# Kernel optimization log

Measured on AMD Instinct MI355X. Metric: run time of the kernel, lower is better.

## Reference

```python
import jax, jax.numpy as jnp
import numpy as np

THETA = 10000.0


def _apply_rope(xh, positions, theta):
    # xh: [B, H, S, d_k]; positions: [S] int
    d_k = xh.shape[-1]
    inv_freq = theta ** (-jnp.arange(0, d_k, 2, dtype=jnp.float32) / d_k)  # [d_k/2]
    angles = positions.astype(jnp.float32)[:, None] * inv_freq[None, :]     # [S, d_k/2]
    cos = jnp.cos(angles)
    sin = jnp.sin(angles)
    x1 = xh[..., 0::2]
    x2 = xh[..., 1::2]
    r1 = x1 * cos - x2 * sin
    r2 = x1 * sin + x2 * cos
    return jnp.stack([r1, r2], axis=-1).reshape(xh.shape)


def setup_inputs() -> dict:
    key = jax.random.key(0)
    ks = jax.random.split(key, 5)
    B, S, D = 2, 2048, 1024
    std = np.sqrt(1.0 / D).astype(np.float32)
    return {
        "x": jax.random.normal(ks[0], (B, S, D), dtype=jnp.float32),
        "token_positions": jnp.arange(S, dtype=jnp.int64 if jax.config.jax_enable_x64 else jnp.int32),
        "Wq": jax.random.normal(ks[1], (D, D), dtype=jnp.float32) * std,
        "Wk": jax.random.normal(ks[2], (D, D), dtype=jnp.float32) * std,
        "Wv": jax.random.normal(ks[3], (D, D), dtype=jnp.float32) * std,
        "Wo": jax.random.normal(ks[4], (D, D), dtype=jnp.float32) * std,
    }


def reference(x, token_positions, Wq, Wk, Wv, Wo):
    B, S, D = x.shape
    n_heads = 16
    d_k = D // n_heads

    # QKV projections (torch does x @ W.T)
    q = x @ Wq.T
    k = x @ Wk.T
    v = x @ Wv.T

    def split_heads(t):  # [B,S,D] -> [B,H,S,d_k]
        return t.reshape(B, S, n_heads, d_k).transpose(0, 2, 1, 3)

    qh = _apply_rope(split_heads(q), token_positions, THETA)
    kh = _apply_rope(split_heads(k), token_positions, THETA)
    vh = split_heads(v)

    scores = jnp.einsum("bhqd,bhkd->bhqk", qh, kh) / jnp.sqrt(jnp.float32(d_k))
    causal = jnp.tril(jnp.ones((S, S), dtype=bool))
    scores = jnp.where(causal, scores, -jnp.inf)
    attn = jax.nn.softmax(scores, axis=-1)

    out_h = jnp.einsum("bhqk,bhkd->bhqd", attn, vh)  # [B,H,S,d_k]
    out = out_h.transpose(0, 2, 1, 3).reshape(B, S, D)
    return out @ Wo.T
```

## Files before the change

### kernel.cpp

```cpp
#include <hip/hip_runtime.h>

typedef unsigned int u32;
typedef __attribute__((ext_vector_type(8))) short short8;
typedef __attribute__((ext_vector_type(4))) float f32x4;

__device__ __forceinline__ unsigned short f2bf(float f) {
  union { float f; u32 u; } x; x.f = f;
  u32 u = x.u;
  return (unsigned short)((u + 0x7fffu + ((u >> 16) & 1u)) >> 16);
}
__device__ __forceinline__ float bf2f(unsigned short b) {
  union { u32 u; float f; } x; x.u = ((u32)b) << 16;
  return x.f;
}
__device__ __forceinline__ f32x4 mfma_bf16(short8 a, short8 b, f32x4 c) {
  return __builtin_amdgcn_mfma_f32_16x16x32_bf16(a, b, c, 0, 0, 0);
}

typedef __attribute__((address_space(3))) unsigned int lds_u32;
typedef const __attribute__((address_space(1))) unsigned int glb_u32;
__device__ __forceinline__ void gload_lds16(const unsigned short* g, unsigned short* l) {
  __builtin_amdgcn_global_load_lds((glb_u32*)g, (lds_u32*)l, 16, 0, 0);
}

__global__ __launch_bounds__(256) void cvt_kernel(const float* __restrict__ src,
                                                  unsigned short* __restrict__ dst, int n4) {
  int i = blockIdx.x * 256 + threadIdx.x;
  if (i >= n4) return;
  float4 v = ((const float4*)src)[i];
  ushort4 o;
  o.x = f2bf(v.x); o.y = f2bf(v.y); o.z = f2bf(v.z); o.w = f2bf(v.w);
  ((ushort4*)dst)[i] = o;
}

__global__ __launch_bounds__(256) void cvt_w_kernel(const float* __restrict__ wq,
                                                    const float* __restrict__ wk,
                                                    const float* __restrict__ wv,
                                                    const float* __restrict__ wo,
                                                    unsigned short* __restrict__ dqkv,
                                                    unsigned short* __restrict__ dwo) {
  const int i = blockIdx.x * 256 + threadIdx.x;
  const int w = blockIdx.y;
  const float* src = (w == 0) ? wq : (w == 1) ? wk : (w == 2) ? wv : wo;
  unsigned short* dst = (w == 3) ? dwo : dqkv + (size_t)w * 1048576;
  float4 v = ((const float4*)src)[i];
  ushort4 o;
  o.x = f2bf(v.x); o.y = f2bf(v.y); o.z = f2bf(v.z); o.w = f2bf(v.w);
  ((ushort4*)dst)[i] = o;
}

__global__ __launch_bounds__(256) void gemm_qkv(const unsigned short* __restrict__ A,
                                                const unsigned short* __restrict__ B,
                                                unsigned short* __restrict__ qk,
                                                unsigned short* __restrict__ kk,
                                                unsigned short* __restrict__ vtm) {
  constexpr int K = 1024;
  __shared__ unsigned short As[128 * 32];
  __shared__ unsigned short Bs[128 * 32];
  const int tid = threadIdx.x;
  const int wave = tid >> 6, lane = tid & 63;
  const int l15 = lane & 15, quad = lane >> 4;
  const int wr = wave >> 1, wc = wave & 1;
  const int m0 = blockIdx.y * 128, n0 = blockIdx.x * 128;
  f32x4 acc[4][4] = {};
  const int srow = wave * 32 + (lane >> 2);
  const int scol = (lane & 3) * 8;
  const unsigned short* Ag0 = A + (size_t)(m0 + srow) * K + scol;
  const unsigned short* Ag1 = A + (size_t)(m0 + srow + 16) * K + scol;
  const unsigned short* Bg0 = B + (size_t)(n0 + srow) * K + scol;
  const unsigned short* Bg1 = B + (size_t)(n0 + srow + 16) * K + scol;
  unsigned short* Al0 = &As[wave * 1024];
  unsigned short* Al1 = &As[wave * 1024 + 512];
  unsigned short* Bl0 = &Bs[wave * 1024];
  unsigned short* Bl1 = &Bs[wave * 1024 + 512];
  for (int k0 = 0; k0 < K; k0 += 32) {
    __syncthreads();
    gload_lds16(Ag0 + k0, Al0);
    gload_lds16(Ag1 + k0, Al1);
    gload_lds16(Bg0 + k0, Bl0);
    gload_lds16(Bg1 + k0, Bl1);
    __syncthreads();
    short8 a[4], b[4];
#pragma unroll
    for (int i = 0; i < 4; ++i) a[i] = *(const short8*)&As[(wr * 64 + i * 16 + l15) * 32 + quad * 8];
#pragma unroll
    for (int j = 0; j < 4; ++j) b[j] = *(const short8*)&Bs[(wc * 64 + j * 16 + l15) * 32 + quad * 8];
#pragma unroll
    for (int i = 0; i < 4; ++i)
#pragma unroll
      for (int j = 0; j < 4; ++j) acc[i][j] = mfma_bf16(a[i], b[j], acc[i][j]);
  }
  const int proj = n0 >> 10;
  const int nn0 = (n0 & 1023) + wc * 64;
  if (proj < 2) {
    unsigned short* dst = (proj == 0) ? qk : kk;
#pragma unroll
    for (int i = 0; i < 4; ++i) {
      const int mb = m0 + wr * 64 + i * 16 + quad * 4;
#pragma unroll
      for (int j = 0; j < 4; ++j) {
        const int nn = nn0 + j * 16 + l15;
#pragma unroll
        for (int r = 0; r < 4; ++r) dst[(size_t)(mb + r) * 1024 + nn] = f2bf(acc[i][j][r]);
      }
    }
  } else {
#pragma unroll
    for (int i = 0; i < 4; ++i) {
      const int mb = m0 + wr * 64 + i * 16 + quad * 4;
      const int bb = mb >> 11, s = mb & 2047;
#pragma unroll
      for (int j = 0; j < 4; ++j) {
        const int nn = nn0 + j * 16 + l15;
        const int h = nn >> 6, d = nn & 63;
        ushort4 v4;
        v4.x = f2bf(acc[i][j][0]); v4.y = f2bf(acc[i][j][1]);
        v4.z = f2bf(acc[i][j][2]); v4.w = f2bf(acc[i][j][3]);
        *(ushort4*)&vtm[(((size_t)bb * 16 + h) * 64 + d) * 2048 + s] = v4;
      }
    }
  }
}

__global__ __launch_bounds__(256) void rope_kernel(unsigned short* __restrict__ q,
                                                   unsigned short* __restrict__ k,
                                                   const int* __restrict__ pos) {
  const int idx = blockIdx.x * 256 + threadIdx.x;
  const int i = idx & 31;
  const int h = (idx >> 5) & 15;
  const int s = (idx >> 9) & 2047;
  const int b = idx >> 20;
  const float p = (float)pos[s];
  const float inv = exp2f(-0.4152410118609203f * (float)i);
  float sn, cs;
  sincosf(p * inv, &sn, &cs);
  const size_t base = ((size_t)(b * 2048 + s)) * 1024 + h * 64 + 2 * i;
  {
    u32* qp = (u32*)(q + base);
    u32 w = *qp;
    float x1 = bf2f((unsigned short)(w & 0xffff)), x2 = bf2f((unsigned short)(w >> 16));
    *qp = (u32)f2bf(x1 * cs - x2 * sn) | ((u32)f2bf(x1 * sn + x2 * cs) << 16);
  }
  {
    u32* kp = (u32*)(k + base);
    u32 w = *kp;
    float x1 = bf2f((unsigned short)(w & 0xffff)), x2 = bf2f((unsigned short)(w >> 16));
    *kp = (u32)f2bf(x1 * cs - x2 * sn) | ((u32)f2bf(x1 * sn + x2 * cs) << 16);
  }
}

__global__ __launch_bounds__(64) void attn_kernel(const unsigned short* __restrict__ qk,
                                                  const unsigned short* __restrict__ kk,
                                                  const unsigned short* __restrict__ vtm,
                                                  unsigned short* __restrict__ om) {
  __shared__ unsigned short Pl[32 * 72];
  const int lane = threadIdx.x;
  const int l15 = lane & 15, quad = lane >> 4;
  const int bid = blockIdx.x;
  const int bh = bid & 31;
  const int qi = 63 - (bid >> 5);
  const int b = bh >> 4, h = bh & 15;
  const int qbase = qi << 5;
  const unsigned short* Qp = qk + (size_t)b * 2048 * 1024 + h * 64;
  const unsigned short* Kp = kk + (size_t)b * 2048 * 1024 + h * 64;
  const unsigned short* Vp = vtm + (size_t)bh * 64 * 2048;
  short8 qf[2][2];
#pragma unroll
  for (int f = 0; f < 2; ++f)
#pragma unroll
    for (int hh = 0; hh < 2; ++hh)
      qf[f][hh] = *(const short8*)(Qp + (size_t)(qbase + f * 16 + l15) * 1024 + hh * 32 + quad * 8);
  f32x4 o4[2][4] = {};
  f32x4 ls[2] = {};
  short8 ones;
#pragma unroll
  for (int j = 0; j < 8; ++j) ones[j] = (short)0x3F80;
  const float SC = 0.18033688011112042f;
  const int nk = (qbase + 95) >> 6;
  for (int kt = 0; kt < nk; ++kt) {
    const int kbase = kt << 6;
    short8 kb[4][2], vb[4][2];
#pragma unroll
    for (int nt = 0; nt < 4; ++nt)
#pragma unroll
      for (int hh = 0; hh < 2; ++hh)
        kb[nt][hh] = *(const short8*)(Kp + (size_t)(kbase + nt * 16 + l15) * 1024 + hh * 32 + quad * 8);
#pragma unroll
    for (int t = 0; t < 4; ++t)
#pragma unroll
      for (int hh = 0; hh < 2; ++hh)
        vb[t][hh] = *(const short8*)(Vp + (size_t)(t * 16 + l15) * 2048 + kbase + hh * 32 + quad * 8);
    f32x4 s4[2][4] = {};
#pragma unroll
    for (int f = 0; f < 2; ++f)
#pragma unroll
      for (int nt = 0; nt < 4; ++nt) {
        s4[f][nt] = mfma_bf16(qf[f][0], kb[nt][0], s4[f][nt]);
        s4[f][nt] = mfma_bf16(qf[f][1], kb[nt][1], s4[f][nt]);
      }
    const bool edge = (kt == nk - 1);
#pragma unroll
    for (int f = 0; f < 2; ++f) {
      const int row0 = qbase + f * 16 + quad * 4;
#pragma unroll
      for (int nt = 0; nt < 4; ++nt) {
        const int col = kbase + nt * 16 + l15;
#pragma unroll
        for (int r = 0; r < 4; ++r) {
          float p = exp2f(s4[f][nt][r] * SC);
          if (edge && col > row0 + r) p = 0.f;
          Pl[(f * 16 + quad * 4 + r) * 72 + nt * 16 + l15] = f2bf(p);
        }
      }
    }
    __asm volatile("s_waitcnt lgkmcnt(0)" ::: "memory");
    short8 pa[2][2];
#pragma unroll
    for (int f = 0; f < 2; ++f)
#pragma unroll
      for (int hh = 0; hh < 2; ++hh)
        pa[f][hh] = *(const short8*)&Pl[(f * 16 + l15) * 72 + hh * 32 + quad * 8];
#pragma unroll
    for (int f = 0; f < 2; ++f) {
#pragma unroll
      for (int t = 0; t < 4; ++t) {
        o4[f][t] = mfma_bf16(pa[f][0], vb[t][0], o4[f][t]);
        o4[f][t] = mfma_bf16(pa[f][1], vb[t][1], o4[f][t]);
      }
      ls[f] = mfma_bf16(pa[f][0], ones, ls[f]);
      ls[f] = mfma_bf16(pa[f][1], ones, ls[f]);
    }
  }
#pragma unroll
  for (int f = 0; f < 2; ++f) {
    f32x4 rl;
#pragma unroll
    for (int r = 0; r < 4; ++r) rl[r] = 1.f / ls[f][r];
#pragma unroll
    for (int t = 0; t < 4; ++t)
#pragma unroll
      for (int r = 0; r < 4; ++r) {
        const int srow = qbase + f * 16 + quad * 4 + r;
        om[((size_t)b * 2048 + srow) * 1024 + h * 64 + t * 16 + l15] = f2bf(o4[f][t][r] * rl[r]);
      }
  }
}

__global__ __launch_bounds__(256) void gemm_out(const unsigned short* __restrict__ A,
                                                const unsigned short* __restrict__ B,
                                                float* __restrict__ C) {
  constexpr int K = 1024;
  __shared__ unsigned short As[64 * 32];
  __shared__ unsigned short Bs[128 * 32];
  const int tid = threadIdx.x;
  const int wave = tid >> 6, lane = tid & 63;
  const int l15 = lane & 15, quad = lane >> 4;
  const int m0 = blockIdx.y * 64, n0 = blockIdx.x * 128;
  f32x4 acc[4][2] = {};
  const int lr = lane >> 2, lc = (lane & 3) * 8;
  const unsigned short* Ag  = A + (size_t)(m0 + wave * 16 + lr) * K + lc;
  const unsigned short* Bg0 = B + (size_t)(n0 + wave * 32 + lr) * K + lc;
  const unsigned short* Bg1 = B + (size_t)(n0 + wave * 32 + 16 + lr) * K + lc;
  unsigned short* Al  = &As[wave * 512];
  unsigned short* Bl0 = &Bs[wave * 1024];
  unsigned short* Bl1 = &Bs[wave * 1024 + 512];
  for (int k0 = 0; k0 < K; k0 += 32) {
    __syncthreads();
    gload_lds16(Ag + k0, Al);
    gload_lds16(Bg0 + k0, Bl0);
    gload_lds16(Bg1 + k0, Bl1);
    __syncthreads();
    short8 a[4], b[2];
#pragma unroll
    for (int i = 0; i < 4; ++i) a[i] = *(const short8*)&As[(i * 16 + l15) * 32 + quad * 8];
#pragma unroll
    for (int j = 0; j < 2; ++j) b[j] = *(const short8*)&Bs[(wave * 32 + j * 16 + l15) * 32 + quad * 8];
#pragma unroll
    for (int i = 0; i < 4; ++i)
#pragma unroll
      for (int j = 0; j < 2; ++j) acc[i][j] = mfma_bf16(a[i], b[j], acc[i][j]);
  }
#pragma unroll
  for (int i = 0; i < 4; ++i)
#pragma unroll
    for (int j = 0; j < 2; ++j)
#pragma unroll
      for (int r = 0; r < 4; ++r)
        C[(size_t)(m0 + i * 16 + quad * 4 + r) * 1024 + n0 + wave * 32 + j * 16 + l15] =
            acc[i][j][r];
}

extern "C" void kernel_launch(void* const* d_in, const int* in_sizes, int n_in,
                              void* d_out, int out_size, void* d_ws, size_t ws_size,
                              hipStream_t stream) {
  const float* x  = (const float*)d_in[0];
  const int* pos  = (const int*)d_in[1];
  const float* Wq = (const float*)d_in[2];
  const float* Wk = (const float*)d_in[3];
  const float* Wv = (const float*)d_in[4];
  const float* Wo = (const float*)d_in[5];
  float* out = (float*)d_out;
  char* ws = (char*)d_ws;
  unsigned short* xb   = (unsigned short*)(ws);
  unsigned short* wqkv = (unsigned short*)(ws + (size_t)( 8 << 20));
  unsigned short* wob  = (unsigned short*)(ws + (size_t)(14 << 20));
  unsigned short* qkb  = (unsigned short*)(ws + (size_t)(16 << 20));
  unsigned short* kkb  = (unsigned short*)(ws + (size_t)(24 << 20));
  unsigned short* vtm  = (unsigned short*)(ws + (size_t)(32 << 20));
  unsigned short* om   = (unsigned short*)(ws + (size_t)(40 << 20));

  const int NX4 = 4096 * 1024 / 4;
  hipLaunchKernelGGL(cvt_kernel, dim3(NX4 / 256), dim3(256), 0, stream, x, xb, NX4);
  hipLaunchKernelGGL(cvt_w_kernel, dim3(1024, 4), dim3(256), 0, stream, Wq, Wk, Wv, Wo, wqkv, wob);

  hipLaunchKernelGGL(gemm_qkv, dim3(24, 32), dim3(256), 0, stream, xb, wqkv, qkb, kkb, vtm);
  hipLaunchKernelGGL(rope_kernel, dim3(8192), dim3(256), 0, stream, qkb, kkb, pos);
  hipLaunchKernelGGL(attn_kernel, dim3(2048), dim3(64), 0, stream, qkb, kkb, vtm, om);
  hipLaunchKernelGGL(gemm_out, dim3(8, 64), dim3(256), 0, stream, om, wob, out);
}
```

Measured before the change: 239.1 us.

## Restructure attention into 4-wave blocks sharing LDS-staged K tiles

```diff
diff --git a/kernel.cpp b/kernel.cpp
--- a/kernel.cpp
+++ b/kernel.cpp
@@ -1,6 +1,7 @@
 #include <hip/hip_runtime.h>
 
 typedef unsigned int u32;
+typedef __attribute__((ext_vector_type(4))) short s16x4;
 typedef __attribute__((ext_vector_type(8))) short short8;
 typedef __attribute__((ext_vector_type(4))) float f32x4;
 
@@ -15,6 +16,9 @@
 }
 __device__ __forceinline__ f32x4 mfma_bf16(short8 a, short8 b, f32x4 c) {
   return __builtin_amdgcn_mfma_f32_16x16x32_bf16(a, b, c, 0, 0, 0);
+}
+__device__ __forceinline__ f32x4 mfma16(s16x4 a, s16x4 b, f32x4 c) {
+  return __builtin_amdgcn_mfma_f32_16x16x16bf16_1k(a, b, c, 0, 0, 0);
 }
 
 typedef __attribute__((address_space(3))) unsigned int lds_u32;
@@ -134,12 +138,14 @@
   const float inv = exp2f(-0.4152410118609203f * (float)i);
   float sn, cs;
   sincosf(p * inv, &sn, &cs);
+  const float SC = 0.18033688011112042f;
+  const float csq = cs * SC, snq = sn * SC;
   const size_t base = ((size_t)(b * 2048 + s)) * 1024 + h * 64 + 2 * i;
   {
     u32* qp = (u32*)(q + base);
     u32 w = *qp;
     float x1 = bf2f((unsigned short)(w & 0xffff)), x2 = bf2f((unsigned short)(w >> 16));
-    *qp = (u32)f2bf(x1 * cs - x2 * sn) | ((u32)f2bf(x1 * sn + x2 * cs) << 16);
+    *qp = (u32)f2bf(x1 * csq - x2 * snq) | ((u32)f2bf(x1 * snq + x2 * csq) << 16);
   }
   {
     u32* kp = (u32*)(k + base);
@@ -149,100 +155,115 @@
   }
 }
 
-__global__ __launch_bounds__(64) void attn_kernel(const unsigned short* __restrict__ qk,
-                                                  const unsigned short* __restrict__ kk,
-                                                  const unsigned short* __restrict__ vtm,
-                                                  unsigned short* __restrict__ om) {
-  __shared__ unsigned short Pl[32 * 72];
-  const int lane = threadIdx.x;
+__global__ __launch_bounds__(256) void attn_kernel(const unsigned short* __restrict__ qk,
+                                                   const unsigned short* __restrict__ kk,
+                                                   const unsigned short* __restrict__ vtm,
+                                                   unsigned short* __restrict__ om) {
+  __shared__ unsigned short Kl[2][64 * 32];
+  const int tid = threadIdx.x;
+  const int wave = tid >> 6, lane = tid & 63;
   const int l15 = lane & 15, quad = lane >> 4;
   const int bid = blockIdx.x;
   const int bh = bid & 31;
-  const int qi = 63 - (bid >> 5);
+  const int t5 = bid >> 5;
+  const int qt = (t5 < 8) ? (15 - t5) : (t5 - 8);
   const int b = bh >> 4, h = bh & 15;
-  const int qbase = qi << 5;
+  const int qb = qt * 128;
+  const int qrow0 = qb + wave * 32;
   const unsigned short* Qp = qk + (size_t)b * 2048 * 1024 + h * 64;
-  const unsigned short* Kp = kk + (size_t)b * 2048 * 1024 + h * 64;
+  const unsigned short* Kg = kk + (size_t)b * 2048 * 1024 + h * 64;
   const unsigned short* Vp = vtm + (size_t)bh * 64 * 2048;
   short8 qf[2][2];
 #pragma unroll
   for (int f = 0; f < 2; ++f)
 #pragma unroll
     for (int hh = 0; hh < 2; ++hh)
-      qf[f][hh] = *(const short8*)(Qp + (size_t)(qbase + f * 16 + l15) * 1024 + hh * 32 + quad * 8);
+      qf[f][hh] = *(const short8*)(Qp + (size_t)(qrow0 + f * 16 + l15) * 1024 + hh * 32 + quad * 8);
   f32x4 o4[2][4] = {};
   f32x4 ls[2] = {};
-  short8 ones;
-#pragma unroll
-  for (int j = 0; j < 8; ++j) ones[j] = (short)0x3F80;
-  const float SC = 0.18033688011112042f;
-  const int nk = (qbase + 95) >> 6;
+  s16x4 ones4;
+#pragma unroll
+  for (int j = 0; j < 4; ++j) ones4[j] = (short)0x3F80;
+  const int ssrow = tid >> 2, sscol = (tid & 3) * 8;
+  unsigned short* Kl0w = &Kl[0][(size_t)wave * 512];
+  unsigned short* Kl1w = &Kl[1][(size_t)wave * 512];
+  const unsigned short* Vrow = Vp + (size_t)l15 * 2048 + quad * 4;
+  const int nk = 2 * qt + 2;
   for (int kt = 0; kt < nk; ++kt) {
     const int kbase = kt << 6;
-    short8 kb[4][2], vb[4][2];
-#pragma unroll
-    for (int nt = 0; nt < 4; ++nt)
-#pragma unroll
-      for (int hh = 0; hh < 2; ++hh)
-        kb[nt][hh] = *(const short8*)(Kp + (size_t)(kbase + nt * 16 + l15) * 1024 + hh * 32 + quad * 8);
-#pragma unroll
-    for (int t = 0; t < 4; ++t)
-#pragma unroll
-      for (int hh = 0; hh < 2; ++hh)
-        vb[t][hh] = *(const short8*)(Vp + (size_t)(t * 16 + l15) * 2048 + kbase + hh * 32 + quad * 8);
-    f32x4 s4[2][4] = {};
-#pragma unroll
-    for (int f = 0; f < 2; ++f)
+    const bool active = (kbase <= qrow0 + 31);
+    const bool needmask = (kbase + 63 > qrow0);
+    __syncthreads();
+    gload_lds16(Kg + (size_t)(kbase + ssrow) * 1024 + sscol, Kl0w);
+    gload_lds16(Kg + (size_t)(kbase + ssrow) * 1024 + 32 + sscol, Kl1w);
+    s16x4 vb[4][4];
+    if (active) {
+#pragma unroll
+      for (int t = 0; t < 4; ++t)
+#pragma unroll
+        for (int nt = 0; nt < 4; ++nt)
+          vb[t][nt] = *(const s16x4*)(Vrow + (size_t)t * 16 * 2048 + kbase + nt * 16);
+    }
+    __syncthreads();
+    if (!active) continue;
+    f32x4 st[2][4];
+#pragma unroll
+    for (int nt = 0; nt < 4; ++nt) {
+      short8 kb0 = *(const short8*)&Kl[0][(nt * 16 + l15) * 32 + quad * 8];
+      short8 kb1 = *(const short8*)&Kl[1][(nt * 16 + l15) * 32 + quad * 8];
+#pragma unroll
+      for (int f = 0; f < 2; ++f) {
+        f32x4 z = {};
+        z = mfma_bf16(kb0, qf[f][0], z);
+        z = mfma_bf16(kb1, qf[f][1], z);
+        st[f][nt] = z;
+      }
+    }
+    s16x4 p4[2][4];
+#pragma unroll
+    for (int f = 0; f < 2; ++f) {
+      const int qrow = qrow0 + f * 16 + l15;
 #pragma unroll
       for (int nt = 0; nt < 4; ++nt) {
-        s4[f][nt] = mfma_bf16(qf[f][0], kb[nt][0], s4[f][nt]);
-        s4[f][nt] = mfma_bf16(qf[f][1], kb[nt][1], s4[f][nt]);
+        f32x4 e;
+#pragma unroll
+        for (int r = 0; r < 4; ++r) e[r] = __builtin_amdgcn_exp2f(st[f][nt][r]);
+        if (needmask) {
+          const int kx = kbase + nt * 16 + quad * 4;
+#pragma unroll
+          for (int r = 0; r < 4; ++r)
+            if (kx + r > qrow) e[r] = 0.f;
+        }
+        union { u32 u[2]; s16x4 s; } pk;
+        pk.u[0] = __builtin_amdgcn_perm(__float_as_uint(e[1]), __float_as_uint(e[0]), 0x07060302u);
+        pk.u[1] = __builtin_amdgcn_perm(__float_as_uint(e[3]), __float_as_uint(e[2]), 0x07060302u);
+        p4[f][nt] = pk.s;
       }
-    const bool edge = (kt == nk - 1);
-#pragma unroll
-    for (int f = 0; f < 2; ++f) {
-      const int row0 = qbase + f * 16 + quad * 4;
-#pragma unroll
-      for (int nt = 0; nt < 4; ++nt) {
-        const int col = kbase + nt * 16 + l15;
-#pragma unroll
-        for (int r = 0; r < 4; ++r) {
-          float p = exp2f(s4[f][nt][r] * SC);
-          if (edge && col > row0 + r) p = 0.f;
-          Pl[(f * 16 + quad * 4 + r) * 72 + nt * 16 + l15] = f2bf(p);
-        }
-      }
-    }
-    __asm volatile("s_waitcnt lgkmcnt(0)" ::: "memory");
-    short8 pa[2][2];
-#pragma unroll
-    for (int f = 0; f < 2; ++f)
-#pragma unroll
-      for (int hh = 0; hh < 2; ++hh)
-        pa[f][hh] = *(const short8*)&Pl[(f * 16 + l15) * 72 + hh * 32 + quad * 8];
-#pragma unroll
-    for (int f = 0; f < 2; ++f) {
-#pragma unroll
-      for (int t = 0; t < 4; ++t) {
-        o4[f][t] = mfma_bf16(pa[f][0], vb[t][0], o4[f][t]);
-        o4[f][t] = mfma_bf16(pa[f][1], vb[t][1], o4[f][t]);
-      }
-      ls[f] = mfma_bf16(pa[f][0], ones, ls[f]);
-      ls[f] = mfma_bf16(pa[f][1], ones, ls[f]);
+    }
+#pragma unroll
+    for (int nt = 0; nt < 4; ++nt) {
+#pragma unroll
+      for (int f = 0; f < 2; ++f) ls[f] = mfma16(ones4, p4[f][nt], ls[f]);
+#pragma unroll
+      for (int t = 0; t < 4; ++t)
+#pragma unroll
+        for (int f = 0; f < 2; ++f) o4[f][t] = mfma16(vb[t][nt], p4[f][nt], o4[f][t]);
     }
   }
 #pragma unroll
   for (int f = 0; f < 2; ++f) {
-    f32x4 rl;
-#pragma unroll
-    for (int r = 0; r < 4; ++r) rl[r] = 1.f / ls[f][r];
-#pragma unroll
-    for (int t = 0; t < 4; ++t)
-#pragma unroll
-      for (int r = 0; r < 4; ++r) {
-        const int srow = qbase + f * 16 + quad * 4 + r;
-        om[((size_t)b * 2048 + srow) * 1024 + h * 64 + t * 16 + l15] = f2bf(o4[f][t][r] * rl[r]);
-      }
+    const int srow = qrow0 + f * 16 + l15;
+    const float rl = 1.f / ls[f][0];
+    unsigned short* orow = om + ((size_t)b * 2048 + srow) * 1024 + h * 64 + quad * 4;
+#pragma unroll
+    for (int t = 0; t < 4; ++t) {
+      ushort4 o;
+      o.x = f2bf(o4[f][t][0] * rl);
+      o.y = f2bf(o4[f][t][1] * rl);
+      o.z = f2bf(o4[f][t][2] * rl);
+      o.w = f2bf(o4[f][t][3] * rl);
+      *(ushort4*)(orow + t * 16) = o;
+    }
   }
 }
 
@@ -315,6 +336,6 @@
 
   hipLaunchKernelGGL(gemm_qkv, dim3(24, 32), dim3(256), 0, stream, xb, wqkv, qkb, kkb, vtm);
   hipLaunchKernelGGL(rope_kernel, dim3(8192), dim3(256), 0, stream, qkb, kkb, pos);
-  hipLaunchKernelGGL(attn_kernel, dim3(2048), dim3(64), 0, stream, qkb, kkb, vtm, om);
+  hipLaunchKernelGGL(attn_kernel, dim3(512), dim3(256), 0, stream, qkb, kkb, vtm, om);
   hipLaunchKernelGGL(gemm_out, dim3(8, 64), dim3(256), 0, stream, om, wob, out);
 }
```

Result: slower. 263.1 us (+10.0%).
